# Kernel optimization log

Measured on AMD Instinct MI355X. Metric: run time of the kernel, lower is better.

The kernel has to match this reference:

```python
import jax, jax.numpy as jnp
import numpy as np
from jax import lax

B, N, D = 4, 2048, 1024
MAX_SEQ = 2048
GROUPS = 4  # math.gcd(1024, 4)
LN_EPS = 1e-5


def setup_inputs() -> dict:
    key = jax.random.key(0)
    ks = jax.random.split(key, 12)
    s = 0.02
    return {
        "x": jax.random.normal(ks[0], (B, N, D), jnp.float32),
        "Wq": jax.random.normal(ks[1], (D, D), jnp.float32) * s,
        "Wk": jax.random.normal(ks[2], (D, D), jnp.float32) * s,
        "Wv": jax.random.normal(ks[3], (D, D), jnp.float32) * s,
        "rel_bias": jax.random.normal(ks[4], (1, MAX_SEQ, MAX_SEQ), jnp.float32) * s,
        "conv_w": jax.random.normal(ks[5], (D, D // GROUPS, 3), jnp.float32) * s,
        "conv_b": jnp.zeros((D,), jnp.float32),
        "resg_w": jax.random.normal(ks[6], (D, D), jnp.float32) * s,
        "resg_b": jnp.zeros((D,), jnp.float32),
        "ln_g": jnp.ones((D,), jnp.float32),
        "ln_b": jnp.zeros((D,), jnp.float32),
        "fc1_w": jax.random.normal(ks[7], (D // 2, D), jnp.float32) * s,
        "fc1_b": jnp.zeros((D // 2,), jnp.float32),
        "fc2_w": jax.random.normal(ks[8], (1, D // 2), jnp.float32) * s,
        "fc2_b": jnp.zeros((1,), jnp.float32),
    }


def _forward(x, Wq, Wk, Wv, rel_bias, conv_w, conv_b, resg_w, resg_b,
             ln_g, ln_b, fc1_w, fc1_b, fc2_w, fc2_b):
    b, n, d = x.shape
    scale = 1.0 / jnp.sqrt(jnp.asarray(d, x.dtype))
    q = x @ Wq.T  # [b,n,dk]
    k = x @ Wk.T
    v = x @ Wv.T  # [b,n,dv]
    att = jnp.einsum("bqd,bkd->bqk", q, k) * scale + rel_bias[:, :n, :n]
    causal = jnp.tril(jnp.ones((n, n), bool))
    att = jnp.where(causal, att, jnp.asarray(-jnp.inf, att.dtype))
    att = jax.nn.softmax(att, axis=-1)  # dropout is identity at eval
    att_out = jnp.einsum("bqk,bkd->bqd", att, v)
    # grouped temporal conv over sequence dim: v [b,n,dv] -> NCH [b,dv,n]
    conv = lax.conv_general_dilated(
        v.transpose(0, 2, 1), conv_w, window_strides=(1,), padding=[(1, 1)],
        dimension_numbers=("NCH", "OIH", "NCH"), feature_group_count=GROUPS)
    conv = conv + conv_b[None, :, None]
    out = att_out + conv.transpose(0, 2, 1)
    res = jax.nn.sigmoid(out @ resg_w.T + resg_b)
    out = x + res * out
    mu = out.mean(-1, keepdims=True)
    var = out.var(-1, keepdims=True)
    out = (out - mu) * lax.rsqrt(var + LN_EPS) * ln_g + ln_b
    h = jax.nn.gelu(out @ fc1_w.T + fc1_b, approximate=False)
    return jax.nn.sigmoid(h @ fc2_w.T + fc2_b)


def reference(x, Wq, Wk, Wv, rel_bias, conv_w, conv_b, resg_w, resg_b,
              ln_g, ln_b, fc1_w, fc1_b, fc2_w, fc2_b):
    return _forward(x, Wq, Wk, Wv, rel_bias, conv_w, conv_b, resg_w, resg_b,
                    ln_g, ln_b, fc1_w, fc1_b, fc2_w, fc2_b)
```

## Files before the change

kernel.cpp:

```cpp
#include <hip/hip_runtime.h>
#include <math.h>

#define NSEQ 2048
#define DDIM 1024
#define BSZ  4
#define BM 128
#define BN 128
#define BK 64

typedef short bf16x8 __attribute__((ext_vector_type(8)));
typedef float f32x4 __attribute__((ext_vector_type(4)));
typedef unsigned int u32;
typedef unsigned short u16;

__device__ __forceinline__ u16 f2bf(float f) {
  union { float f; u32 u; } x; x.f = f;
  u32 r = x.u + 0x7FFFu + ((x.u >> 16) & 1u);
  return (u16)(r >> 16);
}
__device__ __forceinline__ float bf2f(u16 h) {
  union { u32 u; float f; } x; x.u = ((u32)h) << 16; return x.f;
}
__device__ __forceinline__ float sigmoidf_(float x) {
  return 1.0f / (1.0f + expf(-x));
}

__device__ __forceinline__ void async_copy16(const u16* g, u16* l) {
  __builtin_amdgcn_global_load_lds(
      (const __attribute__((address_space(1))) u32*)g,
      (__attribute__((address_space(3))) u32*)l, 16, 0, 0);
}

__device__ __forceinline__ void stage_tile(const u16* __restrict__ gsrc, size_t ld,
                                           int k0, u16* lds, int tid) {
  const int wave = tid >> 6, lane = tid & 63;
  const int rr = lane >> 3;
  const int q  = (lane & 7) ^ rr;
#pragma unroll
  for (int j = 0; j < 4; ++j) {
    const int c = j * 4 + wave;
    async_copy16(gsrc + (size_t)(c * 8 + rr) * ld + k0 + q * 8, lds + c * 512);
  }
}

__device__ __forceinline__ void mfma_step(const u16* Al, const u16* Bl,
                                          int wr, int wc, int l16, int quad,
                                          f32x4 acc[4][4]) {
  const int r7 = l16 & 7;
#pragma unroll
  for (int ks = 0; ks < 2; ++ks) {
    const int s = ((ks * 4 + quad) ^ r7) << 3;
    bf16x8 a[4], b[4];
#pragma unroll
    for (int i = 0; i < 4; ++i) {
      a[i] = *(const bf16x8*)(Al + (wr * 64 + i * 16 + l16) * BK + s);
      b[i] = *(const bf16x8*)(Bl + (wc * 64 + i * 16 + l16) * BK + s);
    }
#pragma unroll
    for (int i = 0; i < 4; ++i)
#pragma unroll
      for (int j = 0; j < 4; ++j)
        acc[i][j] = __builtin_amdgcn_mfma_f32_16x16x32_bf16(a[i], b[j], acc[i][j], 0, 0, 0);
  }
}

__device__ __forceinline__ void zero_acc(f32x4 acc[4][4]) {
#pragma unroll
  for (int i = 0; i < 4; ++i)
#pragma unroll
    for (int j = 0; j < 4; ++j) {
      f32x4 z = {0.f, 0.f, 0.f, 0.f};
      acc[i][j] = z;
    }
}

__device__ __forceinline__ void gemm_loop(const u16* A, size_t lda,
                                          const u16* Bt, size_t ldb, int K,
                                          u16* Al, u16* Bl, int tid,
                                          int wr, int wc, int l16, int quad,
                                          f32x4 acc[4][4]) {
  for (int k0 = 0; k0 < K; k0 += BK) {
    __syncthreads();
    stage_tile(A, lda, k0, Al, tid);
    stage_tile(Bt, ldb, k0, Bl, tid);
    __syncthreads();
    mfma_step(Al, Bl, wr, wc, l16, quad, acc);
  }
}

#define ATT_PB 2228224

__global__ __launch_bounds__(256) void k_prep(
    const float* __restrict__ x,  const float* __restrict__ Wq,
    const float* __restrict__ Wk, const float* __restrict__ Wv,
    const float* __restrict__ rw, const float* __restrict__ f1w,
    const float* __restrict__ cw,
    u16* __restrict__ xb,  u16* __restrict__ Wqb, u16* __restrict__ Wkb,
    u16* __restrict__ Wvb, u16* __restrict__ rwb, u16* __restrict__ f1wb,
    u16* __restrict__ cwp, u16* __restrict__ vpad)
{
  const int blk = blockIdx.x, tid = threadIdx.x;
  const float* s; u16* d; int base;
  if (blk < 8192)       { s = x;   d = xb;   base = blk; }
  else if (blk < 9216)  { s = Wq;  d = Wqb;  base = blk - 8192; }
  else if (blk < 10240) { s = Wk;  d = Wkb;  base = blk - 9216; }
  else if (blk < 11264) { s = Wv;  d = Wvb;  base = blk - 10240; }
  else if (blk < 12288) { s = rw;  d = rwb;  base = blk - 11264; }
  else if (blk < 12800) { s = f1w; d = f1wb; base = blk - 12288; }
  else if (blk < 13824) {
    const int o = blk - 12800, i = tid;
#pragma unroll
    for (int tap = 0; tap < 3; ++tap)
      cwp[(size_t)o * 768 + tap * 256 + i] = f2bf(cw[(size_t)o * 768 + i * 3 + tap]);
    return;
  } else {
    const int e = blk - 13824, bb = e >> 1, which = e & 1;
    u16* row = vpad + (size_t)bb * 2050 * 1024 + (which ? (size_t)2049 * 1024 : 0);
    ushort4 z = {0, 0, 0, 0};
    ((ushort4*)row)[tid] = z;
    return;
  }
  const int i = base * 256 + tid;
  const float4 v = ((const float4*)s)[i];
  ushort4 o;
  o.x = f2bf(v.x); o.y = f2bf(v.y); o.z = f2bf(v.z); o.w = f2bf(v.w);
  ((ushort4*)d)[i] = o;
}

__global__ __launch_bounds__(256) void k_qkv(
    const u16* __restrict__ xb, const u16* __restrict__ Wqb,
    const u16* __restrict__ Wkb, const u16* __restrict__ Wvb,
    u16* __restrict__ qb, u16* __restrict__ kb, u16* __restrict__ vpad)
{
  __shared__ u16 Al[BM * BK], Bl[BN * BK];
  const int tid = threadIdx.x, z = blockIdx.z;
  const u16* W = (z == 0) ? Wqb : ((z == 1) ? Wkb : Wvb);
  const int row0 = blockIdx.x * BM, col0 = blockIdx.y * BN;
  const int lane = tid & 63, wave = tid >> 6;
  const int quad = lane >> 4, l16 = lane & 15, wr = wave >> 1, wc = wave & 1;
  f32x4 acc[4][4];
  zero_acc(acc);
  gemm_loop(xb + (size_t)row0 * DDIM, DDIM, W + (size_t)col0 * DDIM, DDIM, DDIM,
            Al, Bl, tid, wr, wc, l16, quad, acc);
#pragma unroll
  for (int mi = 0; mi < 4; ++mi)
#pragma unroll
    for (int r = 0; r < 4; ++r) {
      const int grow = row0 + wr * 64 + mi * 16 + quad * 4 + r;
#pragma unroll
      for (int ni = 0; ni < 4; ++ni) {
        const int gcol = col0 + wc * 64 + ni * 16 + l16;
        const u16 hv = f2bf(acc[mi][ni][r]);
        if (z == 2) {
          const int b = grow >> 11, t = grow & 2047;
          vpad[(size_t)b * 2050 * 1024 + 1024 + (size_t)t * 1024 + gcol] = hv;
        } else {
          (z == 0 ? qb : kb)[(size_t)grow * DDIM + gcol] = hv;
        }
      }
    }
}

__global__ __launch_bounds__(256) void k_vt(const u16* __restrict__ vpad,
                                            u16* __restrict__ vT)
{
  __shared__ u16 tile[64][72];
  const int t0 = blockIdx.x * 64, d0 = blockIdx.y * 64, b = blockIdx.z;
  const int tid = threadIdx.x;
  const u16* vb = vpad + (size_t)b * 2050 * 1024 + 1024;
#pragma unroll
  for (int p = 0; p < 4; ++p) {
    const int r = p * 16 + (tid >> 4), c = (tid & 15) << 2;
    const ushort4 v4 = *(const ushort4*)(vb + (size_t)(t0 + r) * 1024 + d0 + c);
    tile[r][c] = v4.x; tile[r][c + 1] = v4.y; tile[r][c + 2] = v4.z; tile[r][c + 3] = v4.w;
  }
  __syncthreads();
  u16* ob = vT + (size_t)b * DDIM * NSEQ;
#pragma unroll
  for (int p = 0; p < 4; ++p) {
    const int d = p * 16 + (tid >> 4), t = (tid & 15) << 2;
    ushort4 o;
    o.x = tile[t][d]; o.y = tile[t + 1][d]; o.z = tile[t + 2][d]; o.w = tile[t + 3][d];
    *(ushort4*)(ob + (size_t)(d0 + d) * NSEQ + t0 + t) = o;
  }
}

__global__ __launch_bounds__(256) void k_conv(
    const u16* __restrict__ vpad, const u16* __restrict__ cwp,
    const float* __restrict__ cb, u16* __restrict__ convb)
{
  __shared__ u16 Al[BM * BK], Bl[BN * BK];
  const int tid = threadIdx.x;
  const int row0 = blockIdx.x * BM;
  const int col0 = blockIdx.y * BN;
  const int g = col0 >> 8;
  const int b = row0 >> 11, t0 = row0 & 2047;
  const u16* vb = vpad + (size_t)b * 2050 * 1024 + 1024;
  const u16* Bbase = cwp + (size_t)col0 * 768;
  const int lane = tid & 63, wave = tid >> 6;
  const int quad = lane >> 4, l16 = lane & 15, wr = wave >> 1, wc = wave & 1;
  const int rr = lane >> 3;
  const int q  = (lane & 7) ^ rr;
  const int gch = g << 8;
  f32x4 acc[4][4];
  zero_acc(acc);
  for (int k0 = 0; k0 < 768; k0 += BK) {
    __syncthreads();
    const int tap = k0 >> 8;
    const int i0 = k0 & 255;
#pragma unroll
    for (int j = 0; j < 4; ++j) {
      const int c = j * 4 + wave;
      const int r = c * 8 + rr;
      async_copy16(vb + (size_t)(t0 + r - 1 + tap) * 1024 + gch + i0 + q * 8,
                   Al + c * 512);
    }
    stage_tile(Bbase, 768, k0, Bl, tid);
    __syncthreads();
    mfma_step(Al, Bl, wr, wc, l16, quad, acc);
  }
#pragma unroll
  for (int mi = 0; mi < 4; ++mi)
#pragma unroll
    for (int r = 0; r < 4; ++r) {
      const int grow = row0 + wr * 64 + mi * 16 + quad * 4 + r;
#pragma unroll
      for (int ni = 0; ni < 4; ++ni) {
        const int gcol = col0 + wc * 64 + ni * 16 + l16;
        convb[(size_t)grow * DDIM + gcol] = f2bf(cb[gcol] + acc[mi][ni][r]);
      }
    }
}

__global__ __launch_bounds__(256) void k_scores(
    const u16* __restrict__ qb, const u16* __restrict__ kb,
    const float* __restrict__ rb, float* __restrict__ attp)
{
  __shared__ u16 Al[BM * BK], Bl[BN * BK];
  const int b = blockIdx.x, t = blockIdx.y, tid = threadIdx.x;
  int it = 0;
  while ((it + 1) * (it + 2) / 2 <= t) ++it;
  const int jt = t - it * (it + 1) / 2;
  const int row0 = it * BM, col0 = jt * BN;
  const int lane = tid & 63, wave = tid >> 6;
  const int quad = lane >> 4, l16 = lane & 15, wr = wave >> 1, wc = wave & 1;
  f32x4 acc[4][4];
  zero_acc(acc);
  gemm_loop(qb + ((size_t)b * NSEQ + row0) * DDIM, DDIM,
            kb + ((size_t)b * NSEQ + col0) * DDIM, DDIM, DDIM,
            Al, Bl, tid, wr, wc, l16, quad, acc);
  float* abase = attp + (size_t)b * ATT_PB + (size_t)(it * (it + 1) / 2) * 16384;
  const int ldp = (it + 1) * 128;
#pragma unroll
  for (int mi = 0; mi < 4; ++mi)
#pragma unroll
    for (int r = 0; r < 4; ++r) {
      const int ri = wr * 64 + mi * 16 + quad * 4 + r;
      const int gi = row0 + ri;
#pragma unroll
      for (int ni = 0; ni < 4; ++ni) {
        const int j = col0 + wc * 64 + ni * 16 + l16;
        abase[(size_t)ri * ldp + j] =
            acc[mi][ni][r] * 0.03125f + rb[(size_t)gi * NSEQ + j];
      }
    }
}

__global__ __launch_bounds__(256) void k_softmax(const float* __restrict__ attp,
                                                 u16* __restrict__ pp)
{
  const int i = blockIdx.x, b = blockIdx.y;
  const int it = i >> 7;
  const int wlen = (it + 1) << 7;
  const size_t rbase = (size_t)b * ATT_PB +
                       (size_t)(it * (it + 1) / 2) * 16384 + (size_t)(i & 127) * wlen;
  const float* row = attp + rbase;
  u16* orow = pp + rbase;
  const int valid = i + 1;
  const int tid = threadIdx.x;
  const int lane = tid & 63, wid = tid >> 6;

  float v[8];
  float m = -1e30f;
#pragma unroll
  for (int t = 0; t < 8; ++t) {
    const int idx = tid + (t << 8);
    v[t] = (idx < valid) ? row[idx] : -1e30f;
    m = fmaxf(m, v[t]);
  }
#pragma unroll
  for (int off = 32; off; off >>= 1) m = fmaxf(m, __shfl_xor(m, off));
  __shared__ float red[4];
  if (lane == 0) red[wid] = m;
  __syncthreads();
  m = fmaxf(fmaxf(red[0], red[1]), fmaxf(red[2], red[3]));
  __syncthreads();

  float s = 0.f;
#pragma unroll
  for (int t = 0; t < 8; ++t) {
    const int idx = tid + (t << 8);
    float e = (idx < valid) ? expf(v[t] - m) : 0.f;
    v[t] = e;
    s += e;
  }
#pragma unroll
  for (int off = 32; off; off >>= 1) s += __shfl_xor(s, off);
  if (lane == 0) red[wid] = s;
  __syncthreads();
  s = red[0] + red[1] + red[2] + red[3];
  const float inv = 1.0f / s;
#pragma unroll
  for (int t = 0; t < 8; ++t) {
    const int idx = tid + (t << 8);
    if (idx < wlen) orow[idx] = f2bf(v[t] * inv);
  }
}

__global__ __launch_bounds__(256) void k_pv(
    const u16* __restrict__ pp, const u16* __restrict__ vT,
    const u16* __restrict__ convb, u16* __restrict__ buf1b)
{
  __shared__ u16 Al[BM * BK], Bl[BN * BK];
  const int it = blockIdx.x, nt = blockIdx.y, b = blockIdx.z;
  const int tid = threadIdx.x;
  const int row0 = it * BM, col0 = nt * BN;
  const int K = (it + 1) * BM;
  const int lane = tid & 63, wave = tid >> 6;
  const int quad = lane >> 4, l16 = lane & 15, wr = wave >> 1, wc = wave & 1;
  f32x4 acc[4][4];
  zero_acc(acc);
  gemm_loop(pp + (size_t)b * ATT_PB + (size_t)(it * (it + 1) / 2) * 16384, K,
            vT + ((size_t)b * DDIM + col0) * NSEQ, NSEQ, K,
            Al, Bl, tid, wr, wc, l16, quad, acc);
  const size_t obase = (size_t)b * NSEQ * DDIM;
#pragma unroll
  for (int mi = 0; mi < 4; ++mi)
#pragma unroll
    for (int r = 0; r < 4; ++r) {
      const int grow = row0 + wr * 64 + mi * 16 + quad * 4 + r;
#pragma unroll
      for (int ni = 0; ni < 4; ++ni) {
        const int gcol = col0 + wc * 64 + ni * 16 + l16;
        const size_t idx = obase + (size_t)grow * DDIM + gcol;
        buf1b[idx] = f2bf(acc[mi][ni][r] + bf2f(convb[idx]));
      }
    }
}

__global__ __launch_bounds__(256) void k_resgate(
    const u16* __restrict__ buf1b, const u16* __restrict__ rwb,
    const float* __restrict__ rbias, const u16* __restrict__ xb,
    u16* __restrict__ buf2)
{
  __shared__ u16 Al[BM * BK], Bl[BN * BK];
  const int tid = threadIdx.x;
  const int row0 = blockIdx.x * BM, col0 = blockIdx.y * BN;
  const int lane = tid & 63, wave = tid >> 6;
  const int quad = lane >> 4, l16 = lane & 15, wr = wave >> 1, wc = wave & 1;
  f32x4 acc[4][4];
  zero_acc(acc);
  gemm_loop(buf1b + (size_t)row0 * DDIM, DDIM, rwb + (size_t)col0 * DDIM, DDIM,
            DDIM, Al, Bl, tid, wr, wc, l16, quad, acc);
#pragma unroll
  for (int mi = 0; mi < 4; ++mi)
#pragma unroll
    for (int r = 0; r < 4; ++r) {
      const int grow = row0 + wr * 64 + mi * 16 + quad * 4 + r;
#pragma unroll
      for (int ni = 0; ni < 4; ++ni) {
        const int gcol = col0 + wc * 64 + ni * 16 + l16;
        const size_t idx = (size_t)grow * DDIM + gcol;
        const float gate = sigmoidf_(acc[mi][ni][r] + rbias[gcol]);
        buf2[idx] = f2bf(bf2f(xb[idx]) + gate * bf2f(buf1b[idx]));
      }
    }
}

__global__ __launch_bounds__(256) void k_ln(
    const u16* __restrict__ buf, const float* __restrict__ gw,
    const float* __restrict__ gb, u16* __restrict__ outb)
{
  const int row = blockIdx.x;
  const u16* p = buf + (size_t)row * DDIM;
  const int tid = threadIdx.x;
  const int lane = tid & 63, wid = tid >> 6;
  const int c = tid << 2;
  const ushort4 raw = *(const ushort4*)(p + c);
  float4 val;
  val.x = bf2f(raw.x); val.y = bf2f(raw.y); val.z = bf2f(raw.z); val.w = bf2f(raw.w);
  float s = val.x + val.y + val.z + val.w;
  float s2 = val.x * val.x + val.y * val.y + val.z * val.z + val.w * val.w;
#pragma unroll
  for (int off = 32; off; off >>= 1) {
    s += __shfl_xor(s, off);
    s2 += __shfl_xor(s2, off);
  }
  __shared__ float r1[4], r2[4];
  if (lane == 0) { r1[wid] = s; r2[wid] = s2; }
  __syncthreads();
  s = r1[0] + r1[1] + r1[2] + r1[3];
  s2 = r2[0] + r2[1] + r2[2] + r2[3];
  const float mean = s * (1.0f / DDIM);
  const float var = s2 * (1.0f / DDIM) - mean * mean;
  const float rstd = rsqrtf(var + 1e-5f);
  const float4 g4 = *(const float4*)(gw + c);
  const float4 b4 = *(const float4*)(gb + c);
  ushort4 o;
  o.x = f2bf((val.x - mean) * rstd * g4.x + b4.x);
  o.y = f2bf((val.y - mean) * rstd * g4.y + b4.y);
  o.z = f2bf((val.z - mean) * rstd * g4.z + b4.z);
  o.w = f2bf((val.w - mean) * rstd * g4.w + b4.w);
  *(ushort4*)(outb + (size_t)row * DDIM + c) = o;
}

__global__ __launch_bounds__(256) void k_fc1(
    const u16* __restrict__ A, const u16* __restrict__ W,
    const float* __restrict__ bias, u16* __restrict__ h)
{
  __shared__ u16 Al[BM * BK], Bl[BN * BK];
  const int tid = threadIdx.x;
  const int row0 = blockIdx.x * BM, col0 = blockIdx.y * BN;
  const int lane = tid & 63, wave = tid >> 6;
  const int quad = lane >> 4, l16 = lane & 15, wr = wave >> 1, wc = wave & 1;
  f32x4 acc[4][4];
  zero_acc(acc);
  gemm_loop(A + (size_t)row0 * DDIM, DDIM, W + (size_t)col0 * DDIM, DDIM, DDIM,
            Al, Bl, tid, wr, wc, l16, quad, acc);
#pragma unroll
  for (int mi = 0; mi < 4; ++mi)
#pragma unroll
    for (int r = 0; r < 4; ++r) {
      const int grow = row0 + wr * 64 + mi * 16 + quad * 4 + r;
#pragma unroll
      for (int ni = 0; ni < 4; ++ni) {
        const int gcol = col0 + wc * 64 + ni * 16 + l16;
        const float t = acc[mi][ni][r] + bias[gcol];
        h[(size_t)grow * 512 + gcol] =
            f2bf(0.5f * t * (1.0f + erff(t * 0.70710678118654752f)));
      }
    }
}

__global__ __launch_bounds__(256) void k_fc2(
    const u16* __restrict__ h, const float* __restrict__ w,
    const float* __restrict__ b2, float* __restrict__ out)
{
  const int r = blockIdx.x * 4 + (threadIdx.x >> 6);
  const int lane = threadIdx.x & 63;
  const u16* hp = h + (size_t)r * 512;
  float s = 0.f;
#pragma unroll
  for (int t = 0; t < 8; ++t) {
    const int c = lane + t * 64;
    s = fmaf(bf2f(hp[c]), w[c], s);
  }
#pragma unroll
  for (int off = 32; off; off >>= 1) s += __shfl_xor(s, off);
  if (lane == 0) out[r] = sigmoidf_(s + b2[0]);
}

extern "C" void kernel_launch(void* const* d_in, const int* in_sizes, int n_in,
                              void* d_out, int out_size, void* d_ws, size_t ws_size,
                              hipStream_t stream) {
  const float* x    = (const float*)d_in[0];
  const float* Wq   = (const float*)d_in[1];
  const float* Wk   = (const float*)d_in[2];
  const float* Wv   = (const float*)d_in[3];
  const float* rb   = (const float*)d_in[4];
  const float* cw   = (const float*)d_in[5];
  const float* cb   = (const float*)d_in[6];
  const float* rw   = (const float*)d_in[7];
  const float* rbias= (const float*)d_in[8];
  const float* lng  = (const float*)d_in[9];
  const float* lnb  = (const float*)d_in[10];
  const float* f1w  = (const float*)d_in[11];
  const float* f1b  = (const float*)d_in[12];
  const float* f2w  = (const float*)d_in[13];
  const float* f2b  = (const float*)d_in[14];
  float* out = (float*)d_out;
  char* w8 = (char*)d_ws;

  u16* xb    = (u16*)(w8 + 0);
  u16* Wqb   = (u16*)(w8 + 16777216);
  u16* Wkb   = (u16*)(w8 + 18874368);
  u16* Wvb   = (u16*)(w8 + 20971520);
  u16* rwb   = (u16*)(w8 + 23068672);
  u16* f1wb  = (u16*)(w8 + 25165824);
  u16* cwp   = (u16*)(w8 + 26214400);
  u16* qb    = (u16*)(w8 + 27787264);
  u16* kb    = (u16*)(w8 + 44564480);
  u16* vpad  = (u16*)(w8 + 61341696);
  u16* vT    = (u16*)(w8 + 78135296);
  float* attp= (float*)(w8 + 94912512);
  u16* convb = (u16*)(w8 + 130564096);
  u16* pp    = (u16*)(w8 + 27787264);
  u16* buf1b = (u16*)(w8 + 45613056);
  u16* buf2  = (u16*)(w8 + 94912512);
  u16* ln16  = (u16*)(w8 + 78135296);
  u16* h     = (u16*)(w8 + 112746496);

  k_prep   <<<dim3(13832),     256, 0, stream>>>(x, Wq, Wk, Wv, rw, f1w, cw,
                                                 xb, Wqb, Wkb, Wvb, rwb, f1wb,
                                                 cwp, vpad);
  k_qkv    <<<dim3(64, 8, 3),  256, 0, stream>>>(xb, Wqb, Wkb, Wvb, qb, kb, vpad);
  k_vt     <<<dim3(32, 16, 4), 256, 0, stream>>>(vpad, vT);
  k_conv   <<<dim3(64, 8),     256, 0, stream>>>(vpad, cwp, cb, convb);
  k_scores <<<dim3(4, 136),    256, 0, stream>>>(qb, kb, rb, attp);
  k_softmax<<<dim3(NSEQ, BSZ), 256, 0, stream>>>(attp, pp);
  k_pv     <<<dim3(16, 8, 4),  256, 0, stream>>>(pp, vT, convb, buf1b);
  k_resgate<<<dim3(64, 8),     256, 0, stream>>>(buf1b, rwb, rbias, xb, buf2);
  k_ln     <<<dim3(BSZ * NSEQ),256, 0, stream>>>(buf2, lng, lnb, ln16);
  k_fc1    <<<dim3(64, 4),     256, 0, stream>>>(ln16, f1wb, f1b, h);
  k_fc2    <<<dim3(NSEQ),      256, 0, stream>>>(h, f2w, f2b, out);
}
```

Measured before the change: 379.8 us.

## Fuse V transpose into QKV GEMM, fuse fc2 into fc1, swizzle tiles

The QKV GEMM now writes the transposed V directly from registers through shared memory, so the separate transpose kernel and its re-read of V go away. fc1 folds the GELU output straight into the fc2 dot product using row partial sums and atomics into a zeroed output buffer, and a small final kernel applies the bias and sigmoid. That removes the h intermediate and the fc2 kernel. Grouped block swizzling is added to the QKV, resgate and fc1 GEMMs for L2 reuse, and the causal PV kernel launches its longest row tiles first. The cost is float atomics, which make the summation order nondeterministic, plus extra LDS traffic in the V blocks.

```diff
diff --git a/kernel.cpp b/kernel.cpp
--- a/kernel.cpp
+++ b/kernel.cpp
@@ -97,7 +97,7 @@
     const float* __restrict__ cw,
     u16* __restrict__ xb,  u16* __restrict__ Wqb, u16* __restrict__ Wkb,
     u16* __restrict__ Wvb, u16* __restrict__ rwb, u16* __restrict__ f1wb,
-    u16* __restrict__ cwp, u16* __restrict__ vpad)
+    u16* __restrict__ cwp, u16* __restrict__ vpad, float* __restrict__ outz)
 {
   const int blk = blockIdx.x, tid = threadIdx.x;
   const float* s; u16* d; int base;
@@ -113,12 +113,17 @@
     for (int tap = 0; tap < 3; ++tap)
       cwp[(size_t)o * 768 + tap * 256 + i] = f2bf(cw[(size_t)o * 768 + i * 3 + tap]);
     return;
-  } else {
+  } else if (blk < 13832) {
     const int e = blk - 13824, bb = e >> 1, which = e & 1;
     u16* row = vpad + (size_t)bb * 2050 * 1024 + (which ? (size_t)2049 * 1024 : 0);
     ushort4 z = {0, 0, 0, 0};
     ((ushort4*)row)[tid] = z;
     return;
+  } else {
+    const int e = blk - 13832;
+    float4 z = {0.f, 0.f, 0.f, 0.f};
+    ((float4*)outz)[e * 256 + tid] = z;
+    return;
   }
   const int i = base * 256 + tid;
   const float4 v = ((const float4*)s)[i];
@@ -130,18 +135,25 @@
 __global__ __launch_bounds__(256) void k_qkv(
     const u16* __restrict__ xb, const u16* __restrict__ Wqb,
     const u16* __restrict__ Wkb, const u16* __restrict__ Wvb,
-    u16* __restrict__ qb, u16* __restrict__ kb, u16* __restrict__ vpad)
-{
-  __shared__ u16 Al[BM * BK], Bl[BN * BK];
+    u16* __restrict__ qb, u16* __restrict__ kb, u16* __restrict__ vpad,
+    u16* __restrict__ vT)
+{
+  __shared__ __align__(16) u16 SM[BM * BK + BN * BK];
+  u16* Al = SM;
+  u16* Bl = SM + BM * BK;
   const int tid = threadIdx.x, z = blockIdx.z;
   const u16* W = (z == 0) ? Wqb : ((z == 1) ? Wkb : Wvb);
-  const int row0 = blockIdx.x * BM, col0 = blockIdx.y * BN;
+  const int bid = blockIdx.y * 64 + blockIdx.x;
+  const int grp = bid >> 6, loc = bid & 63;
+  const int rowb = grp * 8 + (loc & 7), colb = loc >> 3;
+  const int row0 = rowb * BM, col0 = colb * BN;
   const int lane = tid & 63, wave = tid >> 6;
   const int quad = lane >> 4, l16 = lane & 15, wr = wave >> 1, wc = wave & 1;
   f32x4 acc[4][4];
   zero_acc(acc);
   gemm_loop(xb + (size_t)row0 * DDIM, DDIM, W + (size_t)col0 * DDIM, DDIM, DDIM,
             Al, Bl, tid, wr, wc, l16, quad, acc);
+  const int b = row0 >> 11, t0 = row0 & 2047;
 #pragma unroll
   for (int mi = 0; mi < 4; ++mi)
 #pragma unroll
@@ -152,36 +164,40 @@
         const int gcol = col0 + wc * 64 + ni * 16 + l16;
         const u16 hv = f2bf(acc[mi][ni][r]);
         if (z == 2) {
-          const int b = grow >> 11, t = grow & 2047;
+          const int t = grow & 2047;
           vpad[(size_t)b * 2050 * 1024 + 1024 + (size_t)t * 1024 + gcol] = hv;
         } else {
           (z == 0 ? qb : kb)[(size_t)grow * DDIM + gcol] = hv;
         }
       }
     }
-}
-
-__global__ __launch_bounds__(256) void k_vt(const u16* __restrict__ vpad,
-                                            u16* __restrict__ vT)
-{
-  __shared__ u16 tile[64][72];
-  const int t0 = blockIdx.x * 64, d0 = blockIdx.y * 64, b = blockIdx.z;
-  const int tid = threadIdx.x;
-  const u16* vb = vpad + (size_t)b * 2050 * 1024 + 1024;
-#pragma unroll
-  for (int p = 0; p < 4; ++p) {
-    const int r = p * 16 + (tid >> 4), c = (tid & 15) << 2;
-    const ushort4 v4 = *(const ushort4*)(vb + (size_t)(t0 + r) * 1024 + d0 + c);
-    tile[r][c] = v4.x; tile[r][c + 1] = v4.y; tile[r][c + 2] = v4.z; tile[r][c + 3] = v4.w;
-  }
-  __syncthreads();
-  u16* ob = vT + (size_t)b * DDIM * NSEQ;
-#pragma unroll
-  for (int p = 0; p < 4; ++p) {
-    const int d = p * 16 + (tid >> 4), t = (tid & 15) << 2;
-    ushort4 o;
-    o.x = tile[t][d]; o.y = tile[t + 1][d]; o.z = tile[t + 2][d]; o.w = tile[t + 3][d];
-    *(ushort4*)(ob + (size_t)(d0 + d) * NSEQ + t0 + t) = o;
+  if (z == 2) {
+    u16* tileT = SM;
+    const int tq = (tid & 15) << 2;
+#pragma unroll
+    for (int p = 0; p < 2; ++p) {
+      __syncthreads();
+      if (wr == p) {
+#pragma unroll
+        for (int mi = 0; mi < 4; ++mi)
+#pragma unroll
+          for (int r = 0; r < 4; ++r) {
+            const int tloc = mi * 16 + quad * 4 + r;
+#pragma unroll
+            for (int ni = 0; ni < 4; ++ni) {
+              const int d = wc * 64 + ni * 16 + l16;
+              tileT[d * 66 + tloc] = f2bf(acc[mi][ni][r]);
+            }
+          }
+      }
+      __syncthreads();
+#pragma unroll
+      for (int k = 0; k < 8; ++k) {
+        const int d = (k << 4) + (tid >> 4);
+        const ushort4 o = *(const ushort4*)(tileT + d * 66 + tq);
+        *(ushort4*)(vT + ((size_t)b * DDIM + col0 + d) * NSEQ + t0 + p * 64 + tq) = o;
+      }
+    }
   }
 }
 
@@ -322,7 +338,7 @@
     const u16* __restrict__ convb, u16* __restrict__ buf1b)
 {
   __shared__ u16 Al[BM * BK], Bl[BN * BK];
-  const int it = blockIdx.x, nt = blockIdx.y, b = blockIdx.z;
+  const int it = 15 - blockIdx.x, nt = blockIdx.y, b = blockIdx.z;
   const int tid = threadIdx.x;
   const int row0 = it * BM, col0 = nt * BN;
   const int K = (it + 1) * BM;
@@ -355,7 +371,9 @@
 {
   __shared__ u16 Al[BM * BK], Bl[BN * BK];
   const int tid = threadIdx.x;
-  const int row0 = blockIdx.x * BM, col0 = blockIdx.y * BN;
+  const int bid = blockIdx.y * 64 + blockIdx.x;
+  const int grp = bid >> 6, loc = bid & 63;
+  const int row0 = (grp * 8 + (loc & 7)) * BM, col0 = (loc >> 3) * BN;
   const int lane = tid & 63, wave = tid >> 6;
   const int quad = lane >> 4, l16 = lane & 15, wr = wave >> 1, wc = wave & 1;
   f32x4 acc[4][4];
@@ -416,48 +434,50 @@
 
 __global__ __launch_bounds__(256) void k_fc1(
     const u16* __restrict__ A, const u16* __restrict__ W,
-    const float* __restrict__ bias, u16* __restrict__ h)
+    const float* __restrict__ bias, const float* __restrict__ w2,
+    float* __restrict__ outacc)
 {
   __shared__ u16 Al[BM * BK], Bl[BN * BK];
   const int tid = threadIdx.x;
-  const int row0 = blockIdx.x * BM, col0 = blockIdx.y * BN;
+  const int bid = blockIdx.y * 64 + blockIdx.x;
+  const int grp = bid >> 5, loc = bid & 31;
+  const int row0 = (grp * 8 + (loc & 7)) * BM, col0 = (loc >> 3) * BN;
   const int lane = tid & 63, wave = tid >> 6;
   const int quad = lane >> 4, l16 = lane & 15, wr = wave >> 1, wc = wave & 1;
   f32x4 acc[4][4];
   zero_acc(acc);
   gemm_loop(A + (size_t)row0 * DDIM, DDIM, W + (size_t)col0 * DDIM, DDIM, DDIM,
             Al, Bl, tid, wr, wc, l16, quad, acc);
+  float w4[4], b4[4];
+#pragma unroll
+  for (int ni = 0; ni < 4; ++ni) {
+    const int gcol = col0 + wc * 64 + ni * 16 + l16;
+    w4[ni] = w2[gcol];
+    b4[ni] = bias[gcol];
+  }
 #pragma unroll
   for (int mi = 0; mi < 4; ++mi)
 #pragma unroll
     for (int r = 0; r < 4; ++r) {
       const int grow = row0 + wr * 64 + mi * 16 + quad * 4 + r;
+      float part = 0.f;
 #pragma unroll
       for (int ni = 0; ni < 4; ++ni) {
-        const int gcol = col0 + wc * 64 + ni * 16 + l16;
-        const float t = acc[mi][ni][r] + bias[gcol];
-        h[(size_t)grow * 512 + gcol] =
-            f2bf(0.5f * t * (1.0f + erff(t * 0.70710678118654752f)));
-      }
-    }
-}
-
-__global__ __launch_bounds__(256) void k_fc2(
-    const u16* __restrict__ h, const float* __restrict__ w,
-    const float* __restrict__ b2, float* __restrict__ out)
-{
-  const int r = blockIdx.x * 4 + (threadIdx.x >> 6);
-  const int lane = threadIdx.x & 63;
-  const u16* hp = h + (size_t)r * 512;
-  float s = 0.f;
-#pragma unroll
-  for (int t = 0; t < 8; ++t) {
-    const int c = lane + t * 64;
-    s = fmaf(bf2f(hp[c]), w[c], s);
-  }
-#pragma unroll
-  for (int off = 32; off; off >>= 1) s += __shfl_xor(s, off);
-  if (lane == 0) out[r] = sigmoidf_(s + b2[0]);
+        const float t = acc[mi][ni][r] + b4[ni];
+        const float g = 0.5f * t * (1.0f + erff(t * 0.70710678118654752f));
+        part = fmaf(g, w4[ni], part);
+      }
+#pragma unroll
+      for (int off = 1; off < 16; off <<= 1) part += __shfl_xor(part, off, 16);
+      if (l16 == 0) atomicAdd(outacc + grow, part);
+    }
+}
+
+__global__ __launch_bounds__(256) void k_fin(float* __restrict__ out,
+                                             const float* __restrict__ b2)
+{
+  const int i = blockIdx.x * 256 + threadIdx.x;
+  out[i] = sigmoidf_(out[i] + b2[0]);
 }
 
 extern "C" void kernel_launch(void* const* d_in, const int* in_sizes, int n_in,
@@ -498,19 +518,18 @@
   u16* buf1b = (u16*)(w8 + 45613056);
   u16* buf2  = (u16*)(w8 + 94912512);
   u16* ln16  = (u16*)(w8 + 78135296);
-  u16* h     = (u16*)(w8 + 112746496);
-
-  k_prep   <<<dim3(13832),     256, 0, stream>>>(x, Wq, Wk, Wv, rw, f1w, cw,
+
+  k_prep   <<<dim3(13840),     256, 0, stream>>>(x, Wq, Wk, Wv, rw, f1w, cw,
                                                  xb, Wqb, Wkb, Wvb, rwb, f1wb,
-                                                 cwp, vpad);
-  k_qkv    <<<dim3(64, 8, 3),  256, 0, stream>>>(xb, Wqb, Wkb, Wvb, qb, kb, vpad);
-  k_vt     <<<dim3(32, 16, 4), 256, 0, stream>>>(vpad, vT);
+                                                 cwp, vpad, out);
+  k_qkv    <<<dim3(64, 8, 3),  256, 0, stream>>>(xb, Wqb, Wkb, Wvb, qb, kb,
+                                                 vpad, vT);
   k_conv   <<<dim3(64, 8),     256, 0, stream>>>(vpad, cwp, cb, convb);
   k_scores <<<dim3(4, 136),    256, 0, stream>>>(qb, kb, rb, attp);
   k_softmax<<<dim3(NSEQ, BSZ), 256, 0, stream>>>(attp, pp);
   k_pv     <<<dim3(16, 8, 4),  256, 0, stream>>>(pp, vT, convb, buf1b);
   k_resgate<<<dim3(64, 8),     256, 0, stream>>>(buf1b, rwb, rbias, xb, buf2);
   k_ln     <<<dim3(BSZ * NSEQ),256, 0, stream>>>(buf2, lng, lnb, ln16);
-  k_fc1    <<<dim3(64, 4),     256, 0, stream>>>(ln16, f1wb, f1b, h);
-  k_fc2    <<<dim3(NSEQ),      256, 0, stream>>>(h, f2w, f2b, out);
-}
+  k_fc1    <<<dim3(64, 4),     256, 0, stream>>>(ln16, f1wb, f1b, f2w, out);
+  k_fin    <<<dim3(32),        256, 0, stream>>>(out, f2b);
+}
```

New measurement: 386.3 us. Within noise of the previous version (+1.7%).
